# Performance work log

Measured on AMD Instinct MI355X. Metric: run time of the kernel, lower is better.

## Reference

```python
import jax, jax.numpy as jnp
import numpy as np

H_D, W_D = 64, 64          # 1024x1024 image / 16 patch size
N = H_D * W_D              # 4096 patches
D = 768                    # DINO ViT-B/16 embed dim
ALPHA = 0.5
K = 100


def setup_inputs() -> dict:
    key = jax.random.key(0)
    k1, k2 = jax.random.split(key)
    out = jax.random.normal(k1, (N, D), dtype=jnp.float32)
    attn_seed = jax.random.randint(k2, (2,), 0, H_D, dtype=jnp.int32)
    return {"out": out, "attn_seed": attn_seed}


def _connected_components(mask):
    """8-connectivity connected components via iterative min-label propagation.
    Background = 0. Foreground pixels get the minimum initial id (+1) of their
    component (same partition as cv2.connectedComponents, different numbering)."""
    fg = mask > 0
    BIG = jnp.int32(N + 1)
    init = jnp.where(fg, jnp.arange(N, dtype=jnp.int32).reshape(H_D, W_D) + 1, BIG)

    def step(l):
        p = jnp.pad(l, 1, constant_values=N + 1)
        m = l
        for dy in (0, 1, 2):          # fixed 3x3 neighborhood, not a data-dim loop
            for dx in (0, 1, 2):
                m = jnp.minimum(m, p[dy:dy + H_D, dx:dx + W_D])
        return jnp.where(fg, m, BIG)

    def cond(st):
        l, prev = st
        return jnp.any(l != prev)

    def body(st):
        l, _ = st
        return step(l), l

    l, _ = jax.lax.while_loop(cond, body, (step(init), init))
    return jnp.where(fg, l, 0)


def reference(out, attn_seed):
    # similarity between all patch features: [N, N]
    sim = out @ out.T
    deg = sim >= 0                                        # degree_matrix (bool)
    # patch with fewest non-negative similarities
    seed_degree_flat = jnp.argmin(deg.sum(axis=0)).astype(jnp.int32)
    seed_degree = jnp.stack([seed_degree_flat // W_D, seed_degree_flat % W_D])
    # blend degree seed with attention seed
    seed_rc = jnp.round(ALPHA * seed_degree + (1.0 - ALPHA) * attn_seed).astype(jnp.int32)
    seed = seed_rc[0] * W_D + seed_rc[1]

    # initial expansion set = patches positively correlated with the seed
    s = deg[seed].astype(jnp.int32)
    s = s.at[seed].set(1)                                 # degree_matrix[seed][seed] = 255 (truthy)
    order = jnp.argsort(-sim[seed])                       # descending
    s = s.at[order[K:]].set(0)                            # keep top-k most similar

    # sequential seed expansion (updates feed into later iterations)
    def step(s, i):
        grows = jnp.sum(sim[i] * (s == 1)) > 0
        s = s.at[i].set(jnp.where(s[i] == 0, 0, jnp.where(grows, 1, 0)))
        return s, None

    s, _ = jax.lax.scan(step, s, jnp.arange(N))

    return _connected_components(s.reshape(H_D, W_D))
```

## Files before the change

kernel.cpp:

```cpp
#include <hip/hip_runtime.h>
#include <cstdint>

#define NP   4096
#define DD   768
#define HD   64
#define WD   64
#define KTOP 100

typedef short bf16x8 __attribute__((ext_vector_type(8)));
typedef float f32x4  __attribute__((ext_vector_type(4)));

__device__ __forceinline__ void gload_lds16(const void* g, void* l) {
    __builtin_amdgcn_global_load_lds(
        (const __attribute__((address_space(1))) unsigned int*)(uintptr_t)g,
        (__attribute__((address_space(3))) unsigned int*)(unsigned int)(uintptr_t)l,
        16, 0, 0);
}

__device__ __forceinline__ unsigned short f2bf_rne(float x) {
    unsigned b = __float_as_uint(x);
    unsigned r = b + 0x7FFFu + ((b >> 16) & 1u);
    return (unsigned short)(r >> 16);
}
__device__ __forceinline__ float bf2f(unsigned short h) {
    return __uint_as_float(((unsigned)h) << 16);
}

__global__ __launch_bounds__(256) void k_split(const float* __restrict__ A,
                                               unsigned short* __restrict__ hi,
                                               unsigned short* __restrict__ lo,
                                               int* __restrict__ counts) {
    if (blockIdx.x < 16) counts[blockIdx.x * 256 + threadIdx.x] = 0;
    int idx = blockIdx.x * 256 + threadIdx.x;
    float4 v = ((const float4*)A)[idx];
    unsigned short h0 = f2bf_rne(v.x), h1 = f2bf_rne(v.y),
                   h2 = f2bf_rne(v.z), h3 = f2bf_rne(v.w);
    unsigned short l0 = f2bf_rne(v.x - bf2f(h0)), l1 = f2bf_rne(v.y - bf2f(h1)),
                   l2 = f2bf_rne(v.z - bf2f(h2)), l3 = f2bf_rne(v.w - bf2f(h3));
    ((ushort4*)hi)[idx] = make_ushort4(h0, h1, h2, h3);
    ((ushort4*)lo)[idx] = make_ushort4(l0, l1, l2, l3);
}

__device__ __forceinline__ void stage_group(const unsigned short* __restrict__ hi,
                                            const unsigned short* __restrict__ lo,
                                            int i0, int j0, int kbase, int tid,
                                            unsigned short* G) {
#pragma unroll
    for (int q = 0; q < 6; ++q) {
        int pp = q * 256 + tid;
        int isB = (pp >= 1024);
        int ppt = isB ? (pp - 1024) : pp;
        int row = ppt >> 3;
        int kcl = (ppt & 7) ^ (row & 7);
        int rbase = isB ? j0 : i0;
        const unsigned short* src =
            ((kcl < 4) ? hi : lo) + (size_t)(rbase + row) * DD + kbase + (kcl & 3) * 8;
        gload_lds16(src, G + pp * 8);
    }
}

__global__ __launch_bounds__(256, 2) void k_gemm(const unsigned short* __restrict__ hi,
                                                 const unsigned short* __restrict__ lo,
                                                 int* __restrict__ counts) {
    __shared__ __align__(16) unsigned short G[2][1536 * 8];

    int t = ((blockIdx.x & 7) * 132) + (blockIdx.x >> 3);
    int pair = t >> 1, h = t & 1;
    int SI = 0, SJ = 0, rem = pair;
    for (;;) {
        int sz = (SI == SJ) ? 36 : 64;
        if (rem < sz) break;
        rem -= sz;
        if (++SJ == 4) { ++SI; SJ = SI; }
    }
    int li, lj;
    if (SI == SJ) {
        int r = 0;
        while (rem >= (8 - r)) { rem -= (8 - r); ++r; }
        li = r; lj = r + rem;
    } else { li = rem >> 3; lj = rem & 7; }
    int bi = SI * 8 + li, bj = SJ * 8 + lj;
    int i0 = bi * 128;
    int j0 = bj * 128 + h * 64;

    int tid = threadIdx.x;
    int lane = tid & 63, w = tid >> 6;
    int wm = w & 1, wn = w >> 1;

    f32x4 acc[4][2];
#pragma unroll
    for (int ti = 0; ti < 4; ++ti)
#pragma unroll
        for (int u = 0; u < 2; ++u) { acc[ti][u][0] = 0.f; acc[ti][u][1] = 0.f;
                                      acc[ti][u][2] = 0.f; acc[ti][u][3] = 0.f; }

    int kcf = lane >> 4;
    int paH[4], paL[4], pbH[2], pbL[2];
#pragma unroll
    for (int tt = 0; tt < 4; ++tt) {
        int arow = wm * 64 + tt * 16 + (lane & 15);
        paH[tt] = arow * 8 + (kcf ^ (arow & 7));
        paL[tt] = arow * 8 + ((kcf + 4) ^ (arow & 7));
    }
#pragma unroll
    for (int u = 0; u < 2; ++u) {
        int brow = wn * 32 + u * 16 + (lane & 15);
        pbH[u] = 1024 + brow * 8 + (kcf ^ (brow & 7));
        pbL[u] = 1024 + brow * 8 + ((kcf + 4) ^ (brow & 7));
    }

    stage_group(hi, lo, i0, j0, 0, tid, G[0]);
    for (int it = 0; it < 24; ++it) {
        int cur = it & 1;
        __syncthreads();
        if (it + 1 < 24)
            stage_group(hi, lo, i0, j0, (it + 1) * 32, tid, G[cur ^ 1]);
        bf16x8 ahi[4], alo[4], bhi[2], blo[2];
#pragma unroll
        for (int tt = 0; tt < 4; ++tt) {
            ahi[tt] = *(const bf16x8*)&G[cur][paH[tt] * 8];
            alo[tt] = *(const bf16x8*)&G[cur][paL[tt] * 8];
        }
#pragma unroll
        for (int u = 0; u < 2; ++u) {
            bhi[u] = *(const bf16x8*)&G[cur][pbH[u] * 8];
            blo[u] = *(const bf16x8*)&G[cur][pbL[u] * 8];
        }
#pragma unroll
        for (int ti = 0; ti < 4; ++ti)
#pragma unroll
            for (int u = 0; u < 2; ++u) {
                acc[ti][u] = __builtin_amdgcn_mfma_f32_16x16x32_bf16(
                    ahi[ti], bhi[u], acc[ti][u], 0, 0, 0);
                acc[ti][u] = __builtin_amdgcn_mfma_f32_16x16x32_bf16(
                    alo[ti], bhi[u], acc[ti][u], 0, 0, 0);
                acc[ti][u] = __builtin_amdgcn_mfma_f32_16x16x32_bf16(
                    ahi[ti], blo[u], acc[ti][u], 0, 0, 0);
            }
    }

    __syncthreads();
    int* colc = (int*)&G[0][0];
    int* rowc = ((int*)&G[0][0]) + 64;
    if (tid < 192) ((int*)&G[0][0])[tid] = 0;
    __syncthreads();

    int nl = lane & 15;
    int rg = lane >> 4;
    int cc[2] = {0, 0};
#pragma unroll
    for (int ti = 0; ti < 4; ++ti)
#pragma unroll
        for (int u = 0; u < 2; ++u) {
            f32x4 a = acc[ti][u];
            cc[u] += ((a[0] >= 0.f) ? 1 : 0) + ((a[1] >= 0.f) ? 1 : 0) +
                     ((a[2] >= 0.f) ? 1 : 0) + ((a[3] >= 0.f) ? 1 : 0);
        }
#pragma unroll
    for (int u = 0; u < 2; ++u) {
        int v = cc[u];
        v += __shfl_xor(v, 16);
        v += __shfl_xor(v, 32);
        if (rg == 0) atomicAdd(&colc[wn * 32 + u * 16 + nl], v);
    }
    if (bi != bj) {
#pragma unroll
        for (int ti = 0; ti < 4; ++ti)
#pragma unroll
            for (int g = 0; g < 4; ++g) {
                int rv = ((acc[ti][0][g] >= 0.f) ? 1 : 0) +
                         ((acc[ti][1][g] >= 0.f) ? 1 : 0);
                rv += __shfl_xor(rv, 1);
                rv += __shfl_xor(rv, 2);
                rv += __shfl_xor(rv, 4);
                rv += __shfl_xor(rv, 8);
                if (nl == 0) atomicAdd(&rowc[wm * 64 + ti * 16 + rg * 4 + g], rv);
            }
    }
    __syncthreads();
    if (tid < 64) atomicAdd(&counts[j0 + tid], colc[tid]);
    if (tid < 128 && bi != bj) atomicAdd(&counts[i0 + tid], rowc[tid]);
}

__device__ __forceinline__ int block_sum256(int v, int lane, int w, int* wred) {
#pragma unroll
    for (int o = 1; o < 64; o <<= 1) v += __shfl_xor(v, o);
    if (lane == 0) wred[w] = v;
    __syncthreads();
    int tt = wred[0] + wred[1] + wred[2] + wred[3];
    __syncthreads();
    return tt;
}
__device__ __forceinline__ int block_exscan256(int v, int lane, int w, int* wred,
                                               int* total) {
    int inc = v;
#pragma unroll
    for (int o = 1; o < 64; o <<= 1) { int u = __shfl_up(inc, o); if (lane >= o) inc += u; }
    if (lane == 63) wred[w] = inc;
    __syncthreads();
    int w0 = wred[0], w1 = wred[1], w2 = wred[2], w3 = wred[3];
    int wofs = (w > 0 ? w0 : 0) + (w > 1 ? w1 : 0) + (w > 2 ? w2 : 0);
    *total = w0 + w1 + w2 + w3;
    __syncthreads();
    return wofs + inc - v;
}

__global__ __launch_bounds__(256) void k_seedrow(const float* __restrict__ A,
                                                 const int* __restrict__ counts,
                                                 const int* __restrict__ attn_seed,
                                                 float* __restrict__ simrow,
                                                 int* __restrict__ seedp,
                                                 int* __restrict__ outp) {
    __shared__ int redA[256], redB[256];
    int tid = threadIdx.x, lane = tid & 63, w = tid >> 6;
    int blk = blockIdx.x;

    int bc = 0x7fffffff, bI = 0;
    for (int j = tid; j < NP; j += 256) {
        int c = counts[j];
        if (c < bc) { bc = c; bI = j; }
    }
    redA[tid] = bc; redB[tid] = bI;
    __syncthreads();
    for (int st = 128; st > 0; st >>= 1) {
        if (tid < st) {
            if (redA[tid + st] < redA[tid] ||
                (redA[tid + st] == redA[tid] && redB[tid + st] < redB[tid])) {
                redA[tid] = redA[tid + st];
                redB[tid] = redB[tid + st];
            }
        }
        __syncthreads();
    }
    int flat = redB[0];
    int sr = flat / WD, sc = flat % WD;
    int vr = sr + attn_seed[0];
    int vc = sc + attn_seed[1];
    int rr, rc;
    if ((vr & 1) == 0) rr = vr >> 1;
    else { int m = vr >> 1; rr = (m & 1) ? m + 1 : m; }
    if ((vc & 1) == 0) rc = vc >> 1;
    else { int m = vc >> 1; rc = (m & 1) ? m + 1 : m; }
    int seed = rr * WD + rc;
    if (blk == 0 && tid == 0) seedp[0] = seed;

    float sv[12];
#pragma unroll
    for (int kk = 0; kk < 12; ++kk) sv[kk] = A[(size_t)seed * DD + lane + kk * 64];
    int jbase = blk * 8 + w * 2;
#pragma unroll
    for (int jj = 0; jj < 2; ++jj) {
        int j = jbase + jj;
        float sum = 0.f;
#pragma unroll
        for (int kk = 0; kk < 12; ++kk)
            sum += sv[kk] * A[(size_t)j * DD + lane + kk * 64];
#pragma unroll
        for (int o = 32; o > 0; o >>= 1) sum += __shfl_down(sum, o);
        if (lane == 0) simrow[j] = sum;
    }
    if (blk < 128 && tid < 32) outp[blk * 32 + tid] = 0;
}

__global__ __launch_bounds__(256) void k_subsel(const float* __restrict__ A,
                                                const float* __restrict__ simrow,
                                                const int* __restrict__ seedp,
                                                int* __restrict__ act, int* __restrict__ Mp,
                                                float* __restrict__ subsim) {
    __shared__ int wred[4];
    __shared__ int act_s[128];
    __shared__ float av[DD];
    int tid = threadIdx.x, lane = tid & 63, w = tid >> 6;
    int seed = seedp[0];
    int base = tid * 16;
    unsigned key[16];
#pragma unroll
    for (int n = 0; n < 16; ++n) {
        unsigned b = __float_as_uint(simrow[base + n]);
        key[n] = (b & 0x80000000u) ? ~b : (b | 0x80000000u);
    }
    unsigned prefix = 0;
    for (int bit = 31; bit >= 0; --bit) {
        unsigned cand = prefix | (1u << bit);
        int c = 0;
#pragma unroll
        for (int n = 0; n < 16; ++n) c += (key[n] >= cand) ? 1 : 0;
        int tot = block_sum256(c, lane, w, wred);
        if (tot >= KTOP) prefix = cand;
    }
    unsigned KT = prefix;
    int cgt = 0, ceq = 0;
#pragma unroll
    for (int n = 0; n < 16; ++n) {
        cgt += (key[n] > KT) ? 1 : 0;
        ceq += (key[n] == KT) ? 1 : 0;
    }
    int totgt = block_sum256(cgt, lane, w, wred);
    int slots = KTOP - totgt;
    int dummy;
    int eqrun = block_exscan256(ceq, lane, w, wred, &dummy);
    int flag[16]; int cf = 0;
#pragma unroll
    for (int n = 0; n < 16; ++n) {
        int j = base + n;
        unsigned k = key[n];
        int topk = (k > KT) || (k == KT && eqrun < slots);
        if (k == KT) ++eqrun;
        int f = (topk && (k >= 0x80000000u || j == seed)) ? 1 : 0;
        flag[n] = f; cf += f;
    }
    int M;
    int off = block_exscan256(cf, lane, w, wred, &M);
#pragma unroll
    for (int n = 0; n < 16; ++n)
        if (flag[n]) act_s[off++] = base + n;
    __syncthreads();

    int p = blockIdx.x;
    if (p == 0) {
        if (tid == 0) Mp[0] = M;
        if (tid < M) act[tid] = act_s[tid];
    }
    if (p >= M) return;

    int ip = act_s[p];
    for (int k = tid; k < DD; k += 256) av[k] = A[(size_t)ip * DD + k];
    __syncthreads();
    for (int q = w; q < M; q += 4) {
        int iq = act_s[q];
        float sum = 0.f;
#pragma unroll
        for (int kk = 0; kk < 12; ++kk) {
            int k = lane + kk * 64;
            sum += av[k] * A[(size_t)iq * DD + k];
        }
#pragma unroll
        for (int o = 32; o > 0; o >>= 1) sum += __shfl_down(sum, o);
        if (lane == 0) subsim[p * 128 + q] = sum;
    }
}

__global__ __launch_bounds__(256) void k_fin(const float* __restrict__ subsim,
                                             const int* __restrict__ act,
                                             const int* __restrict__ Mp,
                                             int* __restrict__ outp) {
    __shared__ float ss[128 * 128];
    __shared__ int act_s[128];
    __shared__ int alive[128];
    __shared__ int lab[128];
    __shared__ unsigned char nbr[128][8];
    __shared__ int ncnt[128];
    __shared__ int chg;
    int M = Mp[0];
    int tid = threadIdx.x, lane = tid & 63;

    if (tid < 128) act_s[tid] = (tid < M) ? act[tid] : 0;
    for (int i4 = tid; i4 < M * 32; i4 += 256) {
        int p = i4 >> 5, qb = (i4 & 31) << 2;
        float4 v = ((const float4*)subsim)[i4];
        ss[(qb + 0) * 128 + ((p + qb + 0) & 127)] = v.x;
        ss[(qb + 1) * 128 + ((p + qb + 1) & 127)] = v.y;
        ss[(qb + 2) * 128 + ((p + qb + 2) & 127)] = v.z;
        ss[(qb + 3) * 128 + ((p + qb + 3) & 127)] = v.w;
    }
    __syncthreads();

    if (tid < 64) {
        float S_lo = 0.f, S_hi = 0.f;
        for (int q = 0; q < M; ++q) {
            S_lo += ss[q * 128 + ((lane + q) & 127)];
            S_hi += ss[q * 128 + ((lane + 64 + q) & 127)];
        }
        float al = (lane < M) ? 1.f : 0.f;
        float ah = (lane + 64 < M) ? 1.f : 0.f;
        for (int p = 0; p < M; ++p) {
            float Sp = (p < 64) ? __shfl(S_lo, p) : __shfl(S_hi, p - 64);
            if (!(Sp > 0.f)) {
                S_lo -= ss[p * 128 + ((lane + p) & 127)];
                S_hi -= ss[p * 128 + ((lane + 64 + p) & 127)];
                if (lane == p)      al = 0.f;
                if (lane + 64 == p) ah = 0.f;
            }
        }
        alive[lane]      = (lane < M && al != 0.f) ? 1 : 0;
        alive[lane + 64] = (lane + 64 < M && ah != 0.f) ? 1 : 0;
    }
    __syncthreads();

    if (tid < 128) {
        int a = (tid < M) ? alive[tid] : 0;
        int c = 0;
        if (a) {
            int id = act_s[tid];
            int y = id >> 6, x = id & 63;
            for (int q = 0; q < M; ++q) {
                if (q == tid || !alive[q]) continue;
                int qid = act_s[q];
                int dy = (qid >> 6) - y, dx = (qid & 63) - x;
                if (dy >= -1 && dy <= 1 && dx >= -1 && dx <= 1)
                    nbr[tid][c++] = (unsigned char)q;
            }
        }
        ncnt[tid] = c;
        lab[tid] = a ? tid : 32767;
    }
    __syncthreads();
    while (true) {
        if (tid == 0) chg = 0;
        __syncthreads();
        int local = 0;
        if (tid < M && alive[tid]) {
            int m = lab[tid];
            int nc = ncnt[tid];
            for (int k = 0; k < nc; ++k) { int u = lab[nbr[tid][k]]; if (u < m) m = u; }
            { int u = lab[m]; if (u < m) m = u; }
            { int u = lab[m]; if (u < m) m = u; }
            if (m < lab[tid]) { lab[tid] = m; local = 1; }
        }
        if (local) chg = 1;
        __syncthreads();
        if (chg == 0) break;
        __syncthreads();
    }
    if (tid < M && alive[tid]) outp[act_s[tid]] = act_s[lab[tid]] + 1;
}

extern "C" void kernel_launch(void* const* d_in, const int* in_sizes, int n_in,
                              void* d_out, int out_size, void* d_ws, size_t ws_size,
                              hipStream_t stream) {
    const float* A = (const float*)d_in[0];
    const int* attn = (const int*)d_in[1];
    int* outp = (int*)d_out;

    char* ws = (char*)d_ws;
    int*            counts = (int*)(ws);
    float*          simrow = (float*)(ws + 16384);
    int*            act    = (int*)(ws + 32768);
    int*            Mp     = (int*)(ws + 33280);
    int*            seedp  = (int*)(ws + 33284);
    float*          subsim = (float*)(ws + 33792);
    unsigned short* hi     = (unsigned short*)(ws + 1048576);
    unsigned short* lo     = (unsigned short*)(ws + 1048576 + 6291456);

    k_split  <<<3072, 256, 0, stream>>>(A, hi, lo, counts);
    k_gemm   <<<1056, 256, 0, stream>>>(hi, lo, counts);
    k_seedrow<<<512,  256, 0, stream>>>(A, counts, attn, simrow, seedp, outp);
    k_subsel <<<128,  256, 0, stream>>>(A, simrow, seedp, act, Mp, subsim);
    k_fin    <<<1,    256, 0, stream>>>(subsim, act, Mp, outp);
}
```

Baseline: 184.3 us.

## Use 128x128 tiles with 512 threads and a triple-buffered LDS GEMM pipeline

```diff
diff --git a/kernel.cpp b/kernel.cpp
--- a/kernel.cpp
+++ b/kernel.cpp
@@ -41,32 +41,32 @@
     ((ushort4*)lo)[idx] = make_ushort4(l0, l1, l2, l3);
 }
 
-__device__ __forceinline__ void stage_group(const unsigned short* __restrict__ hi,
-                                            const unsigned short* __restrict__ lo,
-                                            int i0, int j0, int kbase, int tid,
-                                            unsigned short* G) {
-#pragma unroll
-    for (int q = 0; q < 6; ++q) {
-        int pp = q * 256 + tid;
-        int isB = (pp >= 1024);
-        int ppt = isB ? (pp - 1024) : pp;
+__device__ __forceinline__ void stage_half(const unsigned short* __restrict__ hi,
+                                           const unsigned short* __restrict__ lo,
+                                           int i0, int j0, int kbase, int tid,
+                                           int qbase, unsigned short* G) {
+#pragma unroll
+    for (int q = 0; q < 2; ++q) {
+        int pp = (qbase + q) * 512 + tid;
+        int ppt = pp & 1023;
         int row = ppt >> 3;
         int kcl = (ppt & 7) ^ (row & 7);
-        int rbase = isB ? j0 : i0;
+        int rbase = (pp < 1024) ? i0 : j0;
         const unsigned short* src =
             ((kcl < 4) ? hi : lo) + (size_t)(rbase + row) * DD + kbase + (kcl & 3) * 8;
         gload_lds16(src, G + pp * 8);
     }
 }
 
-__global__ __launch_bounds__(256, 2) void k_gemm(const unsigned short* __restrict__ hi,
+__global__ __launch_bounds__(512, 2) void k_gemm(const unsigned short* __restrict__ hi,
                                                  const unsigned short* __restrict__ lo,
                                                  int* __restrict__ counts) {
-    __shared__ __align__(16) unsigned short G[2][1536 * 8];
-
-    int t = ((blockIdx.x & 7) * 132) + (blockIdx.x >> 3);
-    int pair = t >> 1, h = t & 1;
-    int SI = 0, SJ = 0, rem = pair;
+    __shared__ __align__(16) unsigned short G[3][2048 * 8];
+    __shared__ int colc[128];
+    __shared__ int rowc[128];
+
+    int t = ((blockIdx.x & 7) * 66) + (blockIdx.x >> 3);
+    int SI = 0, SJ = 0, rem = t;
     for (;;) {
         int sz = (SI == SJ) ? 36 : 64;
         if (rem < sz) break;
@@ -80,8 +80,7 @@
         li = r; lj = r + rem;
     } else { li = rem >> 3; lj = rem & 7; }
     int bi = SI * 8 + li, bj = SJ * 8 + lj;
-    int i0 = bi * 128;
-    int j0 = bj * 128 + h * 64;
+    int i0 = bi * 128, j0 = bj * 128;
 
     int tid = threadIdx.x;
     int lane = tid & 63, w = tid >> 6;
@@ -109,40 +108,80 @@
         pbL[u] = 1024 + brow * 8 + ((kcf + 4) ^ (brow & 7));
     }
 
-    stage_group(hi, lo, i0, j0, 0, tid, G[0]);
+    stage_half(hi, lo, i0, j0, 0, tid, 0, G[0]);
+    stage_half(hi, lo, i0, j0, 0, tid, 2, G[0]);
+    stage_half(hi, lo, i0, j0, 32, tid, 0, G[1]);
+    stage_half(hi, lo, i0, j0, 32, tid, 2, G[1]);
+    asm volatile("s_waitcnt vmcnt(4)" ::: "memory");
+    __builtin_amdgcn_s_barrier();
+
+    int cur = 0;
     for (int it = 0; it < 24; ++it) {
-        int cur = it & 1;
-        __syncthreads();
-        if (it + 1 < 24)
-            stage_group(hi, lo, i0, j0, (it + 1) * 32, tid, G[cur ^ 1]);
-        bf16x8 ahi[4], alo[4], bhi[2], blo[2];
-#pragma unroll
-        for (int tt = 0; tt < 4; ++tt) {
-            ahi[tt] = *(const bf16x8*)&G[cur][paH[tt] * 8];
-            alo[tt] = *(const bf16x8*)&G[cur][paL[tt] * 8];
-        }
-#pragma unroll
-        for (int u = 0; u < 2; ++u) {
-            bhi[u] = *(const bf16x8*)&G[cur][pbH[u] * 8];
-            blo[u] = *(const bf16x8*)&G[cur][pbL[u] * 8];
-        }
-#pragma unroll
-        for (int ti = 0; ti < 4; ++ti)
-#pragma unroll
-            for (int u = 0; u < 2; ++u) {
-                acc[ti][u] = __builtin_amdgcn_mfma_f32_16x16x32_bf16(
-                    ahi[ti], bhi[u], acc[ti][u], 0, 0, 0);
-                acc[ti][u] = __builtin_amdgcn_mfma_f32_16x16x32_bf16(
-                    alo[ti], bhi[u], acc[ti][u], 0, 0, 0);
-                acc[ti][u] = __builtin_amdgcn_mfma_f32_16x16x32_bf16(
-                    ahi[ti], blo[u], acc[ti][u], 0, 0, 0);
-            }
-    }
-
-    __syncthreads();
-    int* colc = (int*)&G[0][0];
-    int* rowc = ((int*)&G[0][0]) + 64;
-    if (tid < 192) ((int*)&G[0][0])[tid] = 0;
+        unsigned short* Gc = G[cur];
+        int nx = cur + 2; if (nx >= 3) nx -= 3;
+        unsigned short* Gn = G[nx];
+        int kb2 = (it + 2) * 32;
+        bool more = (it + 2) < 24;
+
+        bf16x8 ah0 = *(const bf16x8*)&Gc[paH[0] * 8];
+        bf16x8 al0 = *(const bf16x8*)&Gc[paL[0] * 8];
+        bf16x8 ah1 = *(const bf16x8*)&Gc[paH[1] * 8];
+        bf16x8 al1 = *(const bf16x8*)&Gc[paL[1] * 8];
+        bf16x8 bh0 = *(const bf16x8*)&Gc[pbH[0] * 8];
+        bf16x8 bl0 = *(const bf16x8*)&Gc[pbL[0] * 8];
+        bf16x8 bh1 = *(const bf16x8*)&Gc[pbH[1] * 8];
+        bf16x8 bl1 = *(const bf16x8*)&Gc[pbL[1] * 8];
+        if (more) stage_half(hi, lo, i0, j0, kb2, tid, 0, Gn);
+        __builtin_amdgcn_s_barrier();
+        asm volatile("s_waitcnt lgkmcnt(0)" ::: "memory");
+        __builtin_amdgcn_s_setprio(1);
+        acc[0][0] = __builtin_amdgcn_mfma_f32_16x16x32_bf16(ah0, bh0, acc[0][0], 0, 0, 0);
+        acc[0][0] = __builtin_amdgcn_mfma_f32_16x16x32_bf16(al0, bh0, acc[0][0], 0, 0, 0);
+        acc[0][0] = __builtin_amdgcn_mfma_f32_16x16x32_bf16(ah0, bl0, acc[0][0], 0, 0, 0);
+        acc[0][1] = __builtin_amdgcn_mfma_f32_16x16x32_bf16(ah0, bh1, acc[0][1], 0, 0, 0);
+        acc[0][1] = __builtin_amdgcn_mfma_f32_16x16x32_bf16(al0, bh1, acc[0][1], 0, 0, 0);
+        acc[0][1] = __builtin_amdgcn_mfma_f32_16x16x32_bf16(ah0, bl1, acc[0][1], 0, 0, 0);
+        acc[1][0] = __builtin_amdgcn_mfma_f32_16x16x32_bf16(ah1, bh0, acc[1][0], 0, 0, 0);
+        acc[1][0] = __builtin_amdgcn_mfma_f32_16x16x32_bf16(al1, bh0, acc[1][0], 0, 0, 0);
+        acc[1][0] = __builtin_amdgcn_mfma_f32_16x16x32_bf16(ah1, bl0, acc[1][0], 0, 0, 0);
+        acc[1][1] = __builtin_amdgcn_mfma_f32_16x16x32_bf16(ah1, bh1, acc[1][1], 0, 0, 0);
+        acc[1][1] = __builtin_amdgcn_mfma_f32_16x16x32_bf16(al1, bh1, acc[1][1], 0, 0, 0);
+        acc[1][1] = __builtin_amdgcn_mfma_f32_16x16x32_bf16(ah1, bl1, acc[1][1], 0, 0, 0);
+        __builtin_amdgcn_s_setprio(0);
+        __builtin_amdgcn_s_barrier();
+
+        bf16x8 ah2 = *(const bf16x8*)&Gc[paH[2] * 8];
+        bf16x8 al2 = *(const bf16x8*)&Gc[paL[2] * 8];
+        bf16x8 ah3 = *(const bf16x8*)&Gc[paH[3] * 8];
+        bf16x8 al3 = *(const bf16x8*)&Gc[paL[3] * 8];
+        if (more) {
+            stage_half(hi, lo, i0, j0, kb2, tid, 2, Gn);
+            asm volatile("s_waitcnt vmcnt(4)" ::: "memory");
+        } else {
+            asm volatile("s_waitcnt vmcnt(0)" ::: "memory");
+        }
+        __builtin_amdgcn_s_barrier();
+        asm volatile("s_waitcnt lgkmcnt(0)" ::: "memory");
+        __builtin_amdgcn_s_setprio(1);
+        acc[2][0] = __builtin_amdgcn_mfma_f32_16x16x32_bf16(ah2, bh0, acc[2][0], 0, 0, 0);
+        acc[2][0] = __builtin_amdgcn_mfma_f32_16x16x32_bf16(al2, bh0, acc[2][0], 0, 0, 0);
+        acc[2][0] = __builtin_amdgcn_mfma_f32_16x16x32_bf16(ah2, bl0, acc[2][0], 0, 0, 0);
+        acc[2][1] = __builtin_amdgcn_mfma_f32_16x16x32_bf16(ah2, bh1, acc[2][1], 0, 0, 0);
+        acc[2][1] = __builtin_amdgcn_mfma_f32_16x16x32_bf16(al2, bh1, acc[2][1], 0, 0, 0);
+        acc[2][1] = __builtin_amdgcn_mfma_f32_16x16x32_bf16(ah2, bl1, acc[2][1], 0, 0, 0);
+        acc[3][0] = __builtin_amdgcn_mfma_f32_16x16x32_bf16(ah3, bh0, acc[3][0], 0, 0, 0);
+        acc[3][0] = __builtin_amdgcn_mfma_f32_16x16x32_bf16(al3, bh0, acc[3][0], 0, 0, 0);
+        acc[3][0] = __builtin_amdgcn_mfma_f32_16x16x32_bf16(ah3, bl0, acc[3][0], 0, 0, 0);
+        acc[3][1] = __builtin_amdgcn_mfma_f32_16x16x32_bf16(ah3, bh1, acc[3][1], 0, 0, 0);
+        acc[3][1] = __builtin_amdgcn_mfma_f32_16x16x32_bf16(al3, bh1, acc[3][1], 0, 0, 0);
+        acc[3][1] = __builtin_amdgcn_mfma_f32_16x16x32_bf16(ah3, bl1, acc[3][1], 0, 0, 0);
+        __builtin_amdgcn_s_setprio(0);
+        __builtin_amdgcn_s_barrier();
+
+        ++cur; if (cur == 3) cur = 0;
+    }
+
+    if (tid < 128) { colc[tid] = 0; rowc[tid] = 0; }
     __syncthreads();
 
     int nl = lane & 15;
@@ -178,8 +217,10 @@
             }
     }
     __syncthreads();
-    if (tid < 64) atomicAdd(&counts[j0 + tid], colc[tid]);
-    if (tid < 128 && bi != bj) atomicAdd(&counts[i0 + tid], rowc[tid]);
+    if (tid < 128) {
+        atomicAdd(&counts[j0 + tid], colc[tid]);
+        if (bi != bj) atomicAdd(&counts[i0 + tid], rowc[tid]);
+    }
 }
 
 __device__ __forceinline__ int block_sum256(int v, int lane, int w, int* wred) {
@@ -443,7 +484,7 @@
     unsigned short* lo     = (unsigned short*)(ws + 1048576 + 6291456);
 
     k_split  <<<3072, 256, 0, stream>>>(A, hi, lo, counts);
-    k_gemm   <<<1056, 256, 0, stream>>>(hi, lo, counts);
+    k_gemm   <<<528,  512, 0, stream>>>(hi, lo, counts);
     k_seedrow<<<512,  256, 0, stream>>>(A, counts, attn, simrow, seedp, outp);
     k_subsel <<<128,  256, 0, stream>>>(A, simrow, seedp, act, Mp, subsim);
     k_fin    <<<1,    256, 0, stream>>>(subsim, act, Mp, outp);
```

Measured after the change: 196.1 us. +6.4%, slower.
